# Optimization experiments

Hardware: AMD Instinct MI355X
Metric: run time of the kernel (lower is better)

## Reference

```python
import jax, jax.numpy as jnp
import numpy as np

SEQ, B, IN_DIM = 100, 2048, 64
MID_I, LATENT, V_MID, V_LAT, MID_O, OUT_DIM = 60, 20, 800, 50, 800, 512


def _lstm_cell(x, h, c, wih, whh, bih, bhh):
    # PyTorch gate order: i, f, g, o
    g = x @ wih.T + h @ whh.T + bih + bhh
    i, f, gg, o = jnp.split(g, 4, axis=-1)
    c = jax.nn.sigmoid(f) * c + jax.nn.sigmoid(i) * jnp.tanh(gg)
    h = jax.nn.sigmoid(o) * jnp.tanh(c)
    return h, c


def _lstm_seq(xs, wih, whh, bih, bhh, hid):
    b = xs.shape[1]
    init = (jnp.zeros((b, hid), xs.dtype), jnp.zeros((b, hid), xs.dtype))
    def step(carry, xt):
        h, c = _lstm_cell(xt, carry[0], carry[1], wih, whh, bih, bhh)
        return (h, c), h
    _, outs = jax.lax.scan(step, init, xs)
    return outs  # (seq, B, hid)


def setup_inputs() -> dict:
    key = jax.random.key(0)
    ks = iter(jax.random.split(key, 40))
    w = lambda shape: jax.random.normal(next(ks), shape, jnp.float32) * 0.05
    p = {}
    p['x'] = jax.random.normal(next(ks), (SEQ, B, IN_DIM), jnp.float32)
    p['fc1_wih'] = w((4 * MID_I, IN_DIM)); p['fc1_whh'] = w((4 * MID_I, MID_I))
    p['fc1_bih'] = w((4 * MID_I,)); p['fc1_bhh'] = w((4 * MID_I,))
    p['fc21_wih'] = w((4 * LATENT, MID_I)); p['fc21_whh'] = w((4 * LATENT, LATENT))
    p['fc21_bih'] = w((4 * LATENT,)); p['fc21_bhh'] = w((4 * LATENT,))
    p['lin1_w'] = w((V_MID, LATENT * SEQ)); p['lin1_b'] = w((V_MID,))
    p['lin2_w'] = w((V_LAT, V_MID)); p['lin2_b'] = w((V_LAT,))
    p['idlin_w'] = w((V_LAT, V_LAT)); p['idlin_b'] = w((V_LAT,))
    p['down1_w'] = w((LATENT, V_LAT)); p['down1_b'] = w((LATENT,))
    p['down2_w'] = w((LATENT, OUT_DIM)); p['down2_b'] = w((LATENT,))
    p['l3_wih'] = w((4 * V_LAT, LATENT)); p['l3_whh'] = w((4 * V_LAT, V_LAT))
    p['l3_bih'] = w((4 * V_LAT,)); p['l3_bhh'] = w((4 * V_LAT,))
    p['l4_wih'] = w((4 * MID_O, V_LAT)); p['l4_whh'] = w((4 * MID_O, MID_O))
    p['l4_bih'] = w((4 * MID_O,)); p['l4_bhh'] = w((4 * MID_O,))
    p['l5_wih'] = w((4 * OUT_DIM, MID_O)); p['l5_whh'] = w((4 * OUT_DIM, OUT_DIM))
    p['l5_bih'] = w((4 * OUT_DIM,)); p['l5_bhh'] = w((4 * OUT_DIM,))
    return p


def reference(x, fc1_wih, fc1_whh, fc1_bih, fc1_bhh,
              fc21_wih, fc21_whh, fc21_bih, fc21_bhh,
              lin1_w, lin1_b, lin2_w, lin2_b,
              idlin_w, idlin_b, down1_w, down1_b, down2_w, down2_b,
              l3_wih, l3_whh, l3_bih, l3_bhh,
              l4_wih, l4_whh, l4_bih, l4_bhh,
              l5_wih, l5_whh, l5_bih, l5_bhh):
    seq, b, _ = x.shape
    # encode
    h1 = jax.nn.relu(_lstm_seq(x, fc1_wih, fc1_whh, fc1_bih, fc1_bhh, MID_I))
    out21 = _lstm_seq(h1, fc21_wih, fc21_whh, fc21_bih, fc21_bhh, LATENT)
    flat = jnp.transpose(out21, (1, 2, 0)).reshape(b, -1)  # (B, latent*seq)
    mu = jax.nn.relu(flat @ lin1_w.T + lin1_b)
    mu = jax.nn.relu(mu @ lin2_w.T + lin2_b)  # (B, v_latent)
    # decode
    h_t = mu
    c_t = mu @ idlin_w.T + idlin_b
    out = mu @ down1_w.T + down1_b
    h2 = jnp.zeros((b, MID_O), mu.dtype); c2 = jnp.zeros((b, MID_O), mu.dtype)
    h3 = jnp.zeros((b, OUT_DIM), mu.dtype); c3 = jnp.zeros((b, OUT_DIM), mu.dtype)
    def step(carry, _):
        h_t, c_t, h2, c2, h3, c3, out = carry
        h_t, c_t = _lstm_cell(out, h_t, c_t, l3_wih, l3_whh, l3_bih, l3_bhh)
        h2, c2 = _lstm_cell(h_t, h2, c2, l4_wih, l4_whh, l4_bih, l4_bhh)
        h3, c3 = _lstm_cell(h2, h3, c3, l5_wih, l5_whh, l5_bih, l5_bhh)
        out = h3 @ down2_w.T + down2_b
        return (h_t, c_t, h2, c2, h3, c3, out), h3
    _, muTheta = jax.lax.scan(step, (h_t, c_t, h2, c2, h3, c3, out), None, length=seq)
    return muTheta, mu
```

## Files before the change

kernel.cpp:

```cpp
#include <hip/hip_runtime.h>
#include <cstdint>
#include <cstddef>

#define SEQ     100
#define BATCH   2048
#define IN_DIM  64
#define MID_I   60
#define LATENT  20
#define V_MID   800
#define V_LAT   50
#define MID_O   800
#define OUT_DIM 512

#define KP4  896
#define KP5  1344
#define KPL1 2048

using f32x4  = __attribute__((ext_vector_type(4))) float;
using u16x8  = __attribute__((ext_vector_type(8))) unsigned short;
using bf16x8 = __attribute__((ext_vector_type(8))) __bf16;
typedef _Float16 f16;
typedef _Float16 f16x8 __attribute__((ext_vector_type(8)));

__device__ __forceinline__ unsigned short f2bf(float x){
// ... 41 lines not shown
            for (int i = 0; i < 4; ++i) {
                int idx = threadIdx.x + i * 256;
                int k = idx & 15, m = idx >> 4;
                int gm = m0 + m, gk = k0 + k;
                float v = 0.f;
                if (gm < M && gk < K) v = A[(size_t)gm * K + gk];
                if (RELU_A1 && src == 0) v = fmaxf(v, 0.f);
                As[k][m] = v;
            }
            #pragma unroll
            for (int i = 0; i < 4; ++i) {
                int idx = threadIdx.x + i * 256;
                int k = idx & 15, n = idx >> 4;
                int gn = n0 + n, gk = k0 + k;
                float v = 0.f;
                if (gn < N && gk < K) v = W[(size_t)gn * K + gk];
                Bs[k][n] = v;
            }
            __syncthreads();
            #pragma unroll
            for (int kk = 0; kk < BK; ++kk) {
                float a[4], b[4];
                #pragma unroll
                for (int i = 0; i < 4; ++i) a[i] = As[kk][ty + i * 16];
                #pragma unroll
                for (int j = 0; j < 4; ++j) b[j] = Bs[kk][tx + j * 16];
                #pragma unroll
                for (int i = 0; i < 4; ++i)
                    #pragma unroll
                    for (int j = 0; j < 4; ++j)
                        acc[i][j] += a[i] * b[j];
            }
            __syncthreads();
        }
    }

    #pragma unroll
    for (int i = 0; i < 4; ++i) {
        int gm = m0 + ty + i * 16;
        if (gm >= M) continue;
        #pragma unroll
        for (int j = 0; j < 4; ++j) {
            int gn = n0 + tx + j * 16;
            if (gn >= N) continue;
            float v = acc[i][j];
            if (b1) v += b1[gn];
            if (b2) v += b2[gn];
            if (RELU_OUT) v = fmaxf(v, 0.f);
            C[(size_t)gm * N + gn] = v;
        }
    }
}

__global__ __launch_bounds__(256, 2)
void gemm_lin1(const unsigned short* __restrict__ Ah, const unsigned short* __restrict__ Al,
               const unsigned short* __restrict__ Bh, const unsigned short* __restrict__ Bl,
               int Kp, int Nstore, const float* __restrict__ bi, float* __restrict__ Cout)
{
    __shared__ __align__(16) char smem[32768];
    const int tid  = threadIdx.x;
    const int lane = tid & 63;
    const int wid  = tid >> 6;
    const int m0   = blockIdx.y * 128;
    const int n0   = blockIdx.x * 128;
    const int wr   = (wid >> 1) << 6;
    const int wc   = (wid & 1) << 6;
    const int fr   = lane & 15;
    const int fg   = lane >> 4;
    const int slotR = ((fg ^ (fr & 3)) << 4);

    const int r0 = 32 * wid + (lane >> 2);
    const int sl = (((lane & 3) ^ ((lane >> 2) & 3)) << 3);
    const unsigned short* gA0h = Ah + (size_t)(m0 + r0)      * Kp + sl;
    const unsigned short* gA1h = Ah + (size_t)(m0 + r0 + 16) * Kp + sl;
    const unsigned short* gA0l = Al + (size_t)(m0 + r0)      * Kp + sl;
    const unsigned short* gA1l = Al + (size_t)(m0 + r0 + 16) * Kp + sl;
    const unsigned short* gB0h = Bh + (size_t)(n0 + r0)      * Kp + sl;
    const unsigned short* gB1h = Bh + (size_t)(n0 + r0 + 16) * Kp + sl;
    const unsigned short* gB0l = Bl + (size_t)(n0 + r0)      * Kp + sl;
    const unsigned short* gB1l = Bl + (size_t)(n0 + r0 + 16) * Kp + sl;
    char* lA0h = smem +     0 + (2 * wid    ) * 1024;
    char* lA1h = smem +     0 + (2 * wid + 1) * 1024;
    char* lA0l = smem +  8192 + (2 * wid    ) * 1024;
    char* lA1l = smem +  8192 + (2 * wid + 1) * 1024;
    char* lB0h = smem + 16384 + (2 * wid    ) * 1024;
    char* lB1h = smem + 16384 + (2 * wid + 1) * 1024;
    char* lB0l = smem + 24576 + (2 * wid    ) * 1024;
    char* lB1l = smem + 24576 + (2 * wid + 1) * 1024;

    f32x4 acc[4][4];
    #pragma unroll
    for (int i = 0; i < 4; ++i)
        #pragma unroll
        for (int j = 0; j < 4; ++j) acc[i][j] = (f32x4){0.f, 0.f, 0.f, 0.f};

    for (int k0 = 0; k0 < Kp; k0 += 32) {
        __syncthreads();
        gld16(gA0h + k0, lA0h); gld16(gA1h + k0, lA1h);
        gld16(gA0l + k0, lA0l); gld16(gA1l + k0, lA1l);
        gld16(gB0h + k0, lB0h); gld16(gB1h + k0, lB1h);
        gld16(gB0l + k0, lB0l); gld16(gB1l + k0, lB1l);
        __syncthreads();

        bf16x8 ah[4], al[4];
        #pragma unroll
        for (int i = 0; i < 4; ++i) {
            int ro = (wr + i * 16 + fr) * 64 + slotR;
            ah[i] = *(const bf16x8*)(smem +        ro);
            al[i] = *(const bf16x8*)(smem + 8192 + ro);
        }
        #pragma unroll
        for (int j = 0; j < 4; ++j) {
            int ro = (wc + j * 16 + fr) * 64 + slotR;
            bf16x8 fbh = *(const bf16x8*)(smem + 16384 + ro);
            bf16x8 fbl = *(const bf16x8*)(smem + 24576 + ro);
            #pragma unroll
            for (int i = 0; i < 4; ++i) {
                acc[i][j] = __builtin_amdgcn_mfma_f32_16x16x32_bf16(ah[i], fbh, acc[i][j], 0, 0, 0);
                acc[i][j] = __builtin_amdgcn_mfma_f32_16x16x32_bf16(ah[i], fbl, acc[i][j], 0, 0, 0);
                acc[i][j] = __builtin_amdgcn_mfma_f32_16x16x32_bf16(al[i], fbh, acc[i][j], 0, 0, 0);
            }
        }
    }

    #pragma unroll
    for (int j = 0; j < 4; ++j) {
        int gc = n0 + wc + j * 16 + fr;
        if (gc >= Nstore) continue;
        float badd = bi[gc];
        #pragma unroll
        for (int i = 0; i < 4; ++i)
            #pragma unroll
            for (int r = 0; r < 4; ++r) {
                int gr = m0 + wr + i * 16 + fg * 4 + r;
                float v = fmaxf(acc[i][j][r] + badd, 0.f);
                Cout[(size_t)gr * Nstore + gc] = v;
            }
    }
}

template<int MODE>
__global__ __launch_bounds__(256, 3)
void gemm_dec(const f16* __restrict__ A, const f16* __restrict__ W,
              int Kp, int NK, int H, int NBX,
              const float* __restrict__ bp,
              float* __restrict__ cstate,
              f16* __restrict__ wr1, int st1, int off1,
              f16* __restrict__ wr2, int st2, int off2,
              float* __restrict__ out_t)
{
    __shared__ __align__(16) char smem[49152];
    const int qq      = NBX * 2;
    const int logical = (blockIdx.x & 7) * qq + (blockIdx.x >> 3);
    const int bx = logical >> 4;
    const int by = logical & 15;
    const int m0 = by * 128;
    const int n0 = bx * 128;

    const int tid  = threadIdx.x;
    const int lane = tid & 63;
    const int wid  = tid >> 6;
    const int wm   = wid >> 1;
    const int wn   = wid & 1;
    const int fr   = lane & 15;
    const int fg   = lane >> 4;
    const int swz  = (fg ^ (fr & 3) ^ ((fr >> 2) & 1)) * 16;

    const int rbase = 32 * wid;
    const int lrow  = lane >> 2;
    const int chnk  = (lane & 3) ^ ((lane >> 2) & 3) ^ ((lane >> 4) & 1);
    const f16* sA0 = A + (size_t)(m0 + rbase + lrow)      * Kp + chnk * 8;
    const f16* sA1 = A + (size_t)(m0 + rbase + 16 + lrow) * Kp + chnk * 8;
    const f16* sW0 = W + (size_t)(n0 + rbase + lrow)      * Kp + chnk * 8;
    const f16* sW1 = W + (size_t)(n0 + rbase + 16 + lrow) * Kp + chnk * 8;

    f32x4 acc[4][4];
    #pragma unroll
    for (int i = 0; i < 4; ++i)
        #pragma unroll
        for (int j = 0; j < 4; ++j) acc[i][j] = (f32x4){0.f, 0.f, 0.f, 0.f};

    auto stage = [&](int t, int buf) {
        const int kb = t * 32;
        char* bb = smem + buf * 16384;
        gld16(sA0 + kb, bb + rbase * 64);
        gld16(sA1 + kb, bb + (rbase + 16) * 64);
        gld16(sW0 + kb, bb + 8192 + rbase * 64);
        gld16(sW1 + kb, bb + 8192 + (rbase + 16) * 64);
    };

    stage(0, 0);
    stage(1, 1);

    int buf = 0;
    for (int t = 0; t < NK; ++t) {
        if (t + 1 < NK) asm volatile("s_waitcnt vmcnt(4)" ::: "memory");
        else            asm volatile("s_waitcnt vmcnt(0)" ::: "memory");
        __builtin_amdgcn_s_barrier();
        if (t + 2 < NK) stage(t + 2, (buf + 2) % 3);
        const char* bb = smem + buf * 16384;
        f16x8 af[4];
        #pragma unroll
        for (int i = 0; i < 4; ++i)
            af[i] = *(const f16x8*)(bb + (64 * wm + 16 * i + fr) * 64 + swz);
        #pragma unroll
        for (int j = 0; j < 4; ++j) {
            f16x8 vw = *(const f16x8*)(bb + 8192 + (64 * wn + 16 * j + fr) * 64 + swz);
            #pragma unroll
            for (int i = 0; i < 4; ++i)
                acc[i][j] = __builtin_amdgcn_mfma_f32_16x16x32_f16(af[i], vw, acc[i][j], 0, 0, 0);
        }
        buf = (buf + 1) % 3;
    }

    float* gt = (float*)smem;
    const int u32 = tid & 31;
    const int r8  = tid >> 5;
    const int unit = (n0 >> 2) + u32;
    const f32x4* bp4 = (const f32x4*)bp;
    const f32x4 bv = bp4[unit];

    #pragma unroll
    for (int half = 0; half < 2; ++half) {
        __syncthreads();
        if (wm == half) {
            #pragma unroll
            for (int i = 0; i < 4; ++i)
                #pragma unroll
                for (int j = 0; j < 4; ++j)
                    #pragma unroll
                    for (int r = 0; r < 4; ++r)
                        gt[(16*i + 4*fg + r) * 132 + 64*wn + 16*j + fr] = acc[i][j][r];
        }
        __syncthreads();
        #pragma unroll
        for (int kk = 0; kk < 8; ++kk) {
            const int lr  = 8 * kk + r8;
            const int row = m0 + 64 * half + lr;
            f32x4 g = *(const f32x4*)(gt + lr * 132 + u32 * 4);
            float gi = g[0] + bv[0], gf = g[1] + bv[1];
            float gg = g[2] + bv[2], go = g[3] + bv[3];
            size_t ci = (size_t)row * H + unit;
            float cn = sigm(gf) * cstate[ci] + sigm(gi) * tanh_f(gg);
            float hn = sigm(go) * tanh_f(cn);
            cstate[ci] = cn;
            f16 hh = (f16)hn;
            wr1[(size_t)row * st1 + off1 + unit] = hh;
            if (MODE == 1) wr2[(size_t)row * st2 + off2 + unit] = hh;
            if (MODE == 2) out_t[(size_t)row * H + unit] = hn;
        }
    }
}

__global__ void split_pack_lin1(const float* __restrict__ src,
                                unsigned short* __restrict__ dh, unsigned short* __restrict__ dl)
{
    int idx = blockIdx.x * blockDim.x + threadIdx.x;
    if (idx >= V_MID * LATENT * SEQ) return;
    int n = idx / (LATENT * SEQ), c = idx - n * (LATENT * SEQ);
    int l = c / SEQ, s = c - l * SEQ;
    float x = src[idx];
    unsigned short h = f2bf(x);
    size_t d = (size_t)n * KPL1 + s * LATENT + l;
    dh[d] = h;
    dl[d] = f2bf(x - bf2f(h));
}

__global__ void pack_f16(const float* __restrict__ src, int total, int K, int Kp,
                         int coff, int HU, f16* __restrict__ dh)
{
    int idx = blockIdx.x * blockDim.x + threadIdx.x;
    if (idx >= total) return;
    int n = idx / K, k = idx - n * K;
    int p = (n % HU) * 4 + n / HU;
    dh[(size_t)p * Kp + coff + k] = (f16)src[idx];
}

__global__ void bias_pack(const float* __restrict__ bih, const float* __restrict__ bhh,
                          int H, float* __restrict__ bp)
{
    int idx = blockIdx.x * blockDim.x + threadIdx.x;
    if (idx >= 4 * H) return;
    int g = idx / H, u = idx - g * H;
    bp[u * 4 + g] = bih[idx] + bhh[idx];
}

__global__ __launch_bounds__(256)
void enc_rec1(const float* __restrict__ xp, int T,
              const float* __restrict__ whh,
              float* __restrict__ hbuf, float* __restrict__ cbuf,
              float* __restrict__ h1relu)
{
    __shared__ float Wt[60][240];
    __shared__ float hs[4][60];
    for (int idx = threadIdx.x; idx < 240 * 60; idx += 256) {
        int n = idx / 60, k = idx % 60;
        Wt[k][n] = whh[idx];
    }
    int wid = threadIdx.x >> 6, lane = threadIdx.x & 63;
    int b = blockIdx.x * 4 + wid;
    float h = 0.f, c = 0.f;
    if (lane < 60) {
        h = hbuf[(size_t)b * 60 + lane];
        c = cbuf[(size_t)b * 60 + lane];
        hs[wid][lane] = h;
    }
    __syncthreads();
    for (int t = 0; t < T; ++t) {
        if (lane < 60) {
            const float* xr = xp + ((size_t)t * BATCH + b) * 240;
            float gi = xr[lane], gf = xr[60 + lane], gg = xr[120 + lane], go = xr[180 + lane];
            for (int k = 0; k < 60; ++k) {
                float v = hs[wid][k];
                gi += v * Wt[k][lane];
                gf += v * Wt[k][60 + lane];
                gg += v * Wt[k][120 + lane];
                go += v * Wt[k][180 + lane];
            }
            float cn = sigm(gf) * c + sigm(gi) * tanh_f(gg);
            float hn = sigm(go) * tanh_f(cn);
            c = cn; h = hn;
            h1relu[((size_t)t * BATCH + b) * 60 + lane] = fmaxf(hn, 0.f);
        }
        __syncthreads();
        if (lane < 60) hs[wid][lane] = h;
        __syncthreads();
    }
    if (lane < 60) {
        hbuf[(size_t)b * 60 + lane] = h;
        cbuf[(size_t)b * 60 + lane] = c;
    }
}

__global__ __launch_bounds__(256)
void enc_rec21(const float* __restrict__ xp, int T, int t0,
               const float* __restrict__ whh,
               float* __restrict__ hbuf, float* __restrict__ cbuf,
               unsigned short* __restrict__ fh, unsigned short* __restrict__ fl)
{
    __shared__ float Wt[20][80];
    __shared__ float hs[4][20];
    for (int idx = threadIdx.x; idx < 80 * 20; idx += 256) {
        int n = idx / 20, k = idx % 20;
        Wt[k][n] = whh[idx];
    }
    int wid = threadIdx.x >> 6, lane = threadIdx.x & 63;
    int b = blockIdx.x * 4 + wid;
    float h = 0.f, c = 0.f;
    if (lane < 20) {
        h = hbuf[(size_t)b * 20 + lane];
        c = cbuf[(size_t)b * 20 + lane];
        hs[wid][lane] = h;
    }
    __syncthreads();
    for (int t = 0; t < T; ++t) {
        if (lane < 20) {
            const float* xr = xp + ((size_t)t * BATCH + b) * 80;
            float gi = xr[lane], gf = xr[20 + lane], gg = xr[40 + lane], go = xr[60 + lane];
            for (int k = 0; k < 20; ++k) {
                float v = hs[wid][k];
                gi += v * Wt[k][lane];
                gf += v * Wt[k][20 + lane];
                gg += v * Wt[k][40 + lane];
                go += v * Wt[k][60 + lane];
            }
            float cn = sigm(gf) * c + sigm(gi) * tanh_f(gg);
            float hn = sigm(go) * tanh_f(cn);
            c = cn; h = hn;
            int col = (t0 + t) * 20 + lane;
            unsigned short hh = f2bf(hn);
            fh[(size_t)b * KPL1 + col] = hh;
            fl[(size_t)b * KPL1 + col] = f2bf(hn - bf2f(hh));
        }
        __syncthreads();
        if (lane < 20) hs[wid][lane] = h;
// ... 1 lines not shown
    }
    if (lane < 20) {
        hbuf[(size_t)b * 20 + lane] = h;
        cbuf[(size_t)b * 20 + lane] = c;
    }
}

__global__ __launch_bounds__(256)
void dec_l3(const float* __restrict__ outb,
            const float* __restrict__ wih,
            const float* __restrict__ whh,
            const float* __restrict__ bih, const float* __restrict__ bhh,
            float* __restrict__ h_t, float* __restrict__ c_t,
            f16* __restrict__ a4)
{
    __shared__ float Wt[70][200];
    __shared__ float xin[4][70];
    for (int idx = threadIdx.x; idx < 200 * 20; idx += 256) {
        int n = idx / 20, k = idx % 20;
        Wt[k][n] = wih[idx];
    }
    for (int idx = threadIdx.x; idx < 200 * 50; idx += 256) {
        int n = idx / 50, k = idx % 50;
        Wt[20 + k][n] = whh[idx];
    }
    int wid = threadIdx.x >> 6, lane = threadIdx.x & 63;
    int b = blockIdx.x * 4 + wid;
    if (lane < 20) xin[wid][lane]      = outb[(size_t)b * 20 + lane];
    if (lane < 50) xin[wid][20 + lane] = h_t[(size_t)b * 50 + lane];
    __syncthreads();
    if (lane < 50) {
        float gi = bih[lane] + bhh[lane];
        float gf = bih[50 + lane] + bhh[50 + lane];
        float gg = bih[100 + lane] + bhh[100 + lane];
        float go = bih[150 + lane] + bhh[150 + lane];
        for (int k = 0; k < 70; ++k) {
            float v = xin[wid][k];
            gi += v * Wt[k][lane];
            gf += v * Wt[k][50 + lane];
            gg += v * Wt[k][100 + lane];
            go += v * Wt[k][150 + lane];
        }
        float cold = c_t[(size_t)b * 50 + lane];
        float cn = sigm(gf) * cold + sigm(gi) * tanh_f(gg);
        float hn = sigm(go) * tanh_f(cn);
        c_t[(size_t)b * 50 + lane] = cn;
        h_t[(size_t)b * 50 + lane] = hn;
        a4[(size_t)b * KP4 + lane] = (f16)hn;
    }
}

__global__ __launch_bounds__(512)
void dec_step3(const float* __restrict__ h3prev,
               const float* __restrict__ w2, const float* __restrict__ b2,
               const float* __restrict__ wih, const float* __restrict__ whh,
               const float* __restrict__ bih, const float* __restrict__ bhh,
               float* __restrict__ h_t, float* __restrict__ c_t,
               f16* __restrict__ a4)
{
    __shared__ float w2s[20][512];
    __shared__ float W3[70][200];
    __shared__ float xb[8][80];
    const int tid  = threadIdx.x;
    const int lane = tid & 63;
    const int w    = tid >> 6;
    const int row  = blockIdx.x * 8 + w;

    for (int idx = tid; idx < 20 * 512; idx += 512)
        w2s[idx >> 9][idx & 511] = w2[idx];
    for (int idx = tid; idx < 200 * 20; idx += 512) {
        int n = idx / 20, k = idx - n * 20;
        W3[k][n] = wih[idx];
    }
    for (int idx = tid; idx < 200 * 50; idx += 512) {
        int n = idx / 50, k = idx - n * 50;
        W3[20 + k][n] = whh[idx];
    }
    if (lane < 50) xb[w][20 + lane] = h_t[(size_t)row * 50 + lane];

    float hreg[8];
    const float* hrow = h3prev + (size_t)row * 512;
    #pragma unroll
    for (int c = 0; c < 8; ++c) hreg[c] = hrow[lane + 64 * c];
    __syncthreads();

    #pragma unroll 4
    for (int n = 0; n < 20; ++n) {
        float s = 0.f;
        #pragma unroll
        for (int c = 0; c < 8; ++c) s += hreg[c] * w2s[n][lane + 64 * c];
        #pragma unroll
        for (int o = 32; o; o >>= 1) s += __shfl_xor(s, o);
        if (lane == 0) xb[w][n] = s + b2[n];
    }
    __syncthreads();

    if (lane < 50) {
        const int u = lane;
        float gi = bih[u] + bhh[u];
        float gf = bih[50 + u] + bhh[50 + u];
        float gg = bih[100 + u] + bhh[100 + u];
        float go = bih[150 + u] + bhh[150 + u];
        for (int k = 0; k < 70; ++k) {
            float v = xb[w][k];
            gi += v * W3[k][u];
            gf += v * W3[k][50 + u];
            gg += v * W3[k][100 + u];
            go += v * W3[k][150 + u];
        }
        size_t ci = (size_t)row * 50 + u;
        float cn = sigm(gf) * c_t[ci] + sigm(gi) * tanh_f(gg);
        float hn = sigm(go) * tanh_f(cn);
        c_t[ci] = cn;
        h_t[ci] = hn;
        a4[(size_t)row * KP4 + u] = (f16)hn;
    }
}

extern "C" void kernel_launch(void* const* d_in, const int* in_sizes, int n_in,
                              void* d_out_v, int out_size, void* d_ws, size_t ws_size,
                              hipStream_t stream)
{
    const float* x        = (const float*)d_in[0];
    const float* fc1_wih  = (const float*)d_in[1];
    const float* fc1_whh  = (const float*)d_in[2];
    const float* fc1_bih  = (const float*)d_in[3];
    const float* fc1_bhh  = (const float*)d_in[4];
    const float* fc21_wih = (const float*)d_in[5];
    const float* fc21_whh = (const float*)d_in[6];
    const float* fc21_bih = (const float*)d_in[7];
    const float* fc21_bhh = (const float*)d_in[8];
    const float* lin1_w   = (const float*)d_in[9];
    const float* lin1_b   = (const float*)d_in[10];
    const float* lin2_w   = (const float*)d_in[11];
    const float* lin2_b   = (const float*)d_in[12];
    const float* idlin_w  = (const float*)d_in[13];
    const float* idlin_b  = (const float*)d_in[14];
    const float* down1_w  = (const float*)d_in[15];
    const float* down1_b  = (const float*)d_in[16];
    const float* down2_w  = (const float*)d_in[17];
    const float* down2_b  = (const float*)d_in[18];
    const float* l3_wih   = (const float*)d_in[19];
    const float* l3_whh   = (const float*)d_in[20];
    const float* l3_bih   = (const float*)d_in[21];
    const float* l3_bhh   = (const float*)d_in[22];
    const float* l4_wih   = (const float*)d_in[23];
    const float* l4_whh   = (const float*)d_in[24];
    const float* l4_bih   = (const float*)d_in[25];
    const float* l4_bhh   = (const float*)d_in[26];
    const float* l5_wih   = (const float*)d_in[27];
    const float* l5_whh   = (const float*)d_in[28];
    const float* l5_bih   = (const float*)d_in[29];
    const float* l5_bhh   = (const float*)d_in[30];
    float* out = (float*)d_out_v;

    char* base = (char*)d_ws;
    size_t off = 0;
    auto alloc = [&](size_t bytes) -> void* {
        off = (off + 255) & ~(size_t)255;
        void* p = base + off;
        off += bytes;
        return p;
    };

    size_t us_begin = (off + 255) & ~(size_t)255;
    f16* W4h = (f16*)alloc((size_t)3200 * KP4 * 2);
    f16* W5h = (f16*)alloc((size_t)2048 * KP5 * 2);
    unsigned short* L1h = (unsigned short*)alloc((size_t)896 * KPL1 * 2);
    unsigned short* L1l = (unsigned short*)alloc((size_t)896 * KPL1 * 2);
    unsigned short* Fh  = (unsigned short*)alloc((size_t)BATCH * KPL1 * 2);
    unsigned short* Fl  = (unsigned short*)alloc((size_t)BATCH * KPL1 * 2);
    f16* A4[2]; f16* A5[2];
    for (int p = 0; p < 2; ++p) {
        A4[p] = (f16*)alloc((size_t)BATCH * KP4 * 2);
        A5[p] = (f16*)alloc((size_t)BATCH * KP5 * 2);
    }
    size_t us_end = off;

    size_t fz_begin = (off + 255) & ~(size_t)255;
    float* c2   = (float*)alloc((size_t)BATCH * MID_O * 4);
    float* c3   = (float*)alloc((size_t)BATCH * OUT_DIM * 4);
    float* hb1  = (float*)alloc((size_t)BATCH * MID_I * 4);
    float* cb1  = (float*)alloc((size_t)BATCH * MID_I * 4);
    float* hb21 = (float*)alloc((size_t)BATCH * LATENT * 4);
    float* cb21 = (float*)alloc((size_t)BATCH * LATENT * 4);
    size_t fz_end = off;

    float* bp4   = (float*)alloc((size_t)4 * MID_O * 4);
    float* bp5   = (float*)alloc((size_t)4 * OUT_DIM * 4);
    float* mu1   = (float*)alloc((size_t)BATCH * V_MID * 4);
    float* mu    = (float*)alloc((size_t)BATCH * V_LAT * 4);
    float* h_t   = (float*)alloc((size_t)BATCH * V_LAT * 4);
    float* c_t   = (float*)alloc((size_t)BATCH * V_LAT * 4);
    float* outb  = (float*)alloc((size_t)BATCH * LATENT * 4);
    const int CH = 20;
    float* xp1c  = (float*)alloc((size_t)CH * BATCH * 4 * MID_I * 4);
    float* h1rc  = (float*)alloc((size_t)CH * BATCH * MID_I * 4);
    float* xp21c = (float*)alloc((size_t)CH * BATCH * 4 * LATENT * 4);

    hipMemsetAsync(base + us_begin, 0, us_end - us_begin, stream);
    hipMemsetAsync(base + fz_begin, 0, fz_end - fz_begin, stream);

    pack_f16<<<(3200 * 50  + 255) / 256, 256, 0, stream>>>(l4_wih, 3200 * 50,  50,  KP4, 0,   800, W4h);
    pack_f16<<<(3200 * 800 + 255) / 256, 256, 0, stream>>>(l4_whh, 3200 * 800, 800, KP4, 64,  800, W4h);
    pack_f16<<<(2048 * 800 + 255) / 256, 256, 0, stream>>>(l5_wih, 2048 * 800, 800, KP5, 0,   512, W5h);
    pack_f16<<<(2048 * 512 + 255) / 256, 256, 0, stream>>>(l5_whh, 2048 * 512, 512, KP5, 832, 512, W5h);
    split_pack_lin1<<<(V_MID * LATENT * SEQ + 255) / 256, 256, 0, stream>>>(lin1_w, L1h, L1l);
    bias_pack<<<(4 * MID_O   + 255) / 256, 256, 0, stream>>>(l4_bih, l4_bhh, MID_O,   bp4);
    bias_pack<<<(4 * OUT_DIM + 255) / 256, 256, 0, stream>>>(l5_bih, l5_bhh, OUT_DIM, bp5);

    for (int c0 = 0; c0 < SEQ; c0 += CH) {
        {
            dim3 g((4 * MID_I + BN - 1) / BN, CH * BATCH / BM);
            gemm2k<false, false><<<g, 256, 0, stream>>>(
                x + (size_t)c0 * BATCH * IN_DIM, IN_DIM, nullptr, 0,
                fc1_wih, nullptr, fc1_bih, fc1_bhh, xp1c, CH * BATCH, 4 * MID_I);
        }
        enc_rec1<<<BATCH / 4, 256, 0, stream>>>(xp1c, CH, fc1_whh, hb1, cb1, h1rc);
        {
            dim3 g((4 * LATENT + BN - 1) / BN, CH * BATCH / BM);
            gemm2k<false, false><<<g, 256, 0, stream>>>(
                h1rc, MID_I, nullptr, 0,
                fc21_wih, nullptr, fc21_bih, fc21_bhh, xp21c, CH * BATCH, 4 * LATENT);
        }
        enc_rec21<<<BATCH / 4, 256, 0, stream>>>(xp21c, CH, c0, fc21_whh, hb21, cb21, Fh, Fl);
    }

    {
        dim3 g(7, 16);
        gemm_lin1<<<g, 256, 0, stream>>>(Fh, Fl, L1h, L1l, KPL1, V_MID, lin1_b, mu1);
    }
    {
        dim3 g((V_LAT + BN - 1) / BN, BATCH / BM);
        gemm2k<false, true><<<g, 256, 0, stream>>>(mu1, V_MID, nullptr, 0,
            lin2_w, nullptr, lin2_b, nullptr, mu, BATCH, V_LAT);
    }

    hipMemcpyAsync(h_t, mu, (size_t)BATCH * V_LAT * 4, hipMemcpyDeviceToDevice, stream);
    {
        dim3 g(1, BATCH / BM);
        gemm2k<false, false><<<g, 256, 0, stream>>>(mu, V_LAT, nullptr, 0,
            idlin_w, nullptr, idlin_b, nullptr, c_t, BATCH, V_LAT);
        gemm2k<false, false><<<g, 256, 0, stream>>>(mu, V_LAT, nullptr, 0,
            down1_w, nullptr, down1_b, nullptr, outb, BATCH, LATENT);
    }

    for (int t = 0; t < SEQ; ++t) {
        const int p = t & 1;
        if (t == 0) {
            dec_l3<<<BATCH / 4, 256, 0, stream>>>(outb, l3_wih, l3_whh, l3_bih, l3_bhh,
                                                  h_t, c_t, A4[0]);
        } else {
            dec_step3<<<BATCH / 8, 512, 0, stream>>>(
                out + (size_t)(t - 1) * BATCH * OUT_DIM,
                down2_w, down2_b, l3_wih, l3_whh, l3_bih, l3_bhh,
                h_t, c_t, A4[p]);
        }
        {
            gemm_dec<1><<<dim3(400), 256, 0, stream>>>(
                A4[p], W4h, KP4, KP4 / 32, MID_O, 25, bp4, c2,
                A4[p ^ 1], KP4, 64,
                A5[p], KP5, 0,
                nullptr);
        }
        {
            gemm_dec<2><<<dim3(256), 256, 0, stream>>>(
                A5[p], W5h, KP5, KP5 / 32, OUT_DIM, 16, bp5, c3,
                A5[p ^ 1], KP5, 832,
                nullptr, 0, 0,
                out + (size_t)t * BATCH * OUT_DIM);
        }
    }

    hipMemcpyAsync(out + (size_t)SEQ * BATCH * OUT_DIM, mu,
                   (size_t)BATCH * V_LAT * 4, hipMemcpyDeviceToDevice, stream);
}
```

Measured before the change: 7.671 ms.

## Use split-bf16 MFMA for encoder input GEMMs and retile layer-4 decoder GEMM

The encoder input projections for fc1 and fc21 now run on a generalized split-bf16 (hi/lo) MFMA GEMM instead of the scalar gemm2k. Inputs, weights and the relu'd h1 are pre-split into bf16 pairs, and the two biases are pre-summed. The decoder layer-4 GEMM is retiled to 256x128 blocks with 512 threads and 200 blocks, which halves redundant weight loads per block but uses more LDS and gives fewer blocks. The down2 weight is also stored as f16 in LDS inside dec_step3, which adds small precision loss in the output feedback.

```diff
diff --git a/kernel.cpp b/kernel.cpp
--- a/kernel.cpp
+++ b/kernel.cpp
@@ -117,10 +117,11 @@
     }
 }
 
+template<bool RELU>
 __global__ __launch_bounds__(256, 2)
-void gemm_lin1(const unsigned short* __restrict__ Ah, const unsigned short* __restrict__ Al,
-               const unsigned short* __restrict__ Bh, const unsigned short* __restrict__ Bl,
-               int Kp, int Nstore, const float* __restrict__ bi, float* __restrict__ Cout)
+void gemm_mfma0(const unsigned short* __restrict__ Ah, const unsigned short* __restrict__ Al,
+                const unsigned short* __restrict__ Bh, const unsigned short* __restrict__ Bl,
+                int Kp, int Nstore, const float* __restrict__ bi, float* __restrict__ Cout)
 {
     __shared__ __align__(16) char smem[32768];
     const int tid  = threadIdx.x;
@@ -198,28 +199,26 @@
             #pragma unroll
             for (int r = 0; r < 4; ++r) {
                 int gr = m0 + wr + i * 16 + fg * 4 + r;
-                float v = fmaxf(acc[i][j][r] + badd, 0.f);
+                float v = acc[i][j][r] + badd;
+                if (RELU) v = fmaxf(v, 0.f);
                 Cout[(size_t)gr * Nstore + gc] = v;
             }
     }
 }
 
-template<int MODE>
-__global__ __launch_bounds__(256, 3)
-void gemm_dec(const f16* __restrict__ A, const f16* __restrict__ W,
-              int Kp, int NK, int H, int NBX,
-              const float* __restrict__ bp,
-              float* __restrict__ cstate,
-              f16* __restrict__ wr1, int st1, int off1,
-              f16* __restrict__ wr2, int st2, int off2,
-              float* __restrict__ out_t)
-{
-    __shared__ __align__(16) char smem[49152];
-    const int qq      = NBX * 2;
+__global__ __launch_bounds__(512, 2)
+void gemm_dec4(const f16* __restrict__ A, const f16* __restrict__ W,
+               int Kp, int NK, int H, int NBX,
+               const float* __restrict__ bp, float* __restrict__ cstate,
+               f16* __restrict__ wr1, int st1, int off1,
+               f16* __restrict__ wr2, int st2, int off2)
+{
+    __shared__ __align__(16) char smem[73728];
+    const int qq      = NBX;
     const int logical = (blockIdx.x & 7) * qq + (blockIdx.x >> 3);
-    const int bx = logical >> 4;
-    const int by = logical & 15;
-    const int m0 = by * 128;
+    const int bx = logical >> 3;
+    const int by = logical & 7;
+    const int m0 = by * 256;
     const int n0 = bx * 128;
 
     const int tid  = threadIdx.x;
@@ -232,6 +231,113 @@
     const int swz  = (fg ^ (fr & 3) ^ ((fr >> 2) & 1)) * 16;
 
     const int rbase = 32 * wid;
+    const int rbW   = 16 * wid;
+    const int lrow  = lane >> 2;
+    const int chnk  = (lane & 3) ^ ((lane >> 2) & 3) ^ ((lane >> 4) & 1);
+    const f16* sA0 = A + (size_t)(m0 + rbase + lrow)      * Kp + chnk * 8;
+    const f16* sA1 = A + (size_t)(m0 + rbase + 16 + lrow) * Kp + chnk * 8;
+    const f16* sW  = W + (size_t)(n0 + rbW + lrow)        * Kp + chnk * 8;
+
+    f32x4 acc[4][4];
+    #pragma unroll
+    for (int i = 0; i < 4; ++i)
+        #pragma unroll
+        for (int j = 0; j < 4; ++j) acc[i][j] = (f32x4){0.f, 0.f, 0.f, 0.f};
+
+    auto stage = [&](int t, int buf) {
+        const int kb = t * 32;
+        char* bb = smem + buf * 24576;
+        gld16(sA0 + kb, bb + rbase * 64);
+        gld16(sA1 + kb, bb + (rbase + 16) * 64);
+        gld16(sW  + kb, bb + 16384 + rbW * 64);
+    };
+
+    stage(0, 0);
+    stage(1, 1);
+
+    int buf = 0;
+    for (int t = 0; t < NK; ++t) {
+        if (t + 1 < NK) asm volatile("s_waitcnt vmcnt(3)" ::: "memory");
+        else            asm volatile("s_waitcnt vmcnt(0)" ::: "memory");
+        __builtin_amdgcn_s_barrier();
+        if (t + 2 < NK) stage(t + 2, (buf + 2) % 3);
+        const char* bb = smem + buf * 24576;
+        f16x8 af[4];
+        #pragma unroll
+        for (int i = 0; i < 4; ++i)
+            af[i] = *(const f16x8*)(bb + (64 * wm + 16 * i + fr) * 64 + swz);
+        #pragma unroll
+        for (int j = 0; j < 4; ++j) {
+            f16x8 vw = *(const f16x8*)(bb + 16384 + (64 * wn + 16 * j + fr) * 64 + swz);
+            #pragma unroll
+            for (int i = 0; i < 4; ++i)
+                acc[i][j] = __builtin_amdgcn_mfma_f32_16x16x32_f16(af[i], vw, acc[i][j], 0, 0, 0);
+        }
+        buf = (buf + 1) % 3;
+    }
+
+    float* gt = (float*)smem;
+    const int u32 = tid & 31;
+    const int rr  = tid >> 5;
+    const int unit = (n0 >> 2) + u32;
+    const f32x4 bv = ((const f32x4*)bp)[unit];
+
+    #pragma unroll
+    for (int qp = 0; qp < 4; ++qp) {
+        __syncthreads();
+        if (wm == qp) {
+            #pragma unroll
+            for (int i = 0; i < 4; ++i)
+                #pragma unroll
+                for (int j = 0; j < 4; ++j)
+                    #pragma unroll
+                    for (int r = 0; r < 4; ++r)
+                        gt[(16*i + 4*fg + r) * 132 + 64*wn + 16*j + fr] = acc[i][j][r];
+        }
+        __syncthreads();
+        #pragma unroll
+        for (int kk = 0; kk < 4; ++kk) {
+            const int lr  = 16 * kk + rr;
+            const int row = m0 + 64 * qp + lr;
+            f32x4 g = *(const f32x4*)(gt + lr * 132 + u32 * 4);
+            float gi = g[0] + bv[0], gf = g[1] + bv[1];
+            float gg = g[2] + bv[2], go = g[3] + bv[3];
+            size_t ci = (size_t)row * H + unit;
+            float cn = sigm(gf) * cstate[ci] + sigm(gi) * tanh_f(gg);
+            float hn = sigm(go) * tanh_f(cn);
+            cstate[ci] = cn;
+            f16 hh = (f16)hn;
+            wr1[(size_t)row * st1 + off1 + unit] = hh;
+            wr2[(size_t)row * st2 + off2 + unit] = hh;
+        }
+    }
+}
+
+__global__ __launch_bounds__(256, 3)
+void gemm_dec5(const f16* __restrict__ A, const f16* __restrict__ W,
+               int Kp, int NK, int H, int NBX,
+               const float* __restrict__ bp, float* __restrict__ cstate,
+               f16* __restrict__ wr1, int st1, int off1,
+               float* __restrict__ out_t)
+{
+    __shared__ __align__(16) char smem[49152];
+    const int qq      = NBX * 2;
+    const int logical = (blockIdx.x & 7) * qq + (blockIdx.x >> 3);
+    const int bx = logical >> 4;
+    const int by = logical & 15;
+    const int m0 = by * 128;
+    const int n0 = bx * 128;
+
+    const int tid  = threadIdx.x;
+    const int lane = tid & 63;
+    const int wid  = tid >> 6;
+    const int wm   = wid >> 1;
+    const int wn   = wid & 1;
+    const int fr   = lane & 15;
+    const int fg   = lane >> 4;
+    const int swz  = (fg ^ (fr & 3) ^ ((fr >> 2) & 1)) * 16;
+
+    const int rbase = 32 * wid;
     const int lrow  = lane >> 2;
     const int chnk  = (lane & 3) ^ ((lane >> 2) & 3) ^ ((lane >> 4) & 1);
     const f16* sA0 = A + (size_t)(m0 + rbase + lrow)      * Kp + chnk * 8;
@@ -282,8 +388,7 @@
     const int u32 = tid & 31;
     const int r8  = tid >> 5;
     const int unit = (n0 >> 2) + u32;
-    const f32x4* bp4 = (const f32x4*)bp;
-    const f32x4 bv = bp4[unit];
+    const f32x4 bv = ((const f32x4*)bp)[unit];
 
     #pragma unroll
     for (int half = 0; half < 2; ++half) {
@@ -309,10 +414,8 @@
             float cn = sigm(gf) * cstate[ci] + sigm(gi) * tanh_f(gg);
             float hn = sigm(go) * tanh_f(cn);
             cstate[ci] = cn;
-            f16 hh = (f16)hn;
-            wr1[(size_t)row * st1 + off1 + unit] = hh;
-            if (MODE == 1) wr2[(size_t)row * st2 + off2 + unit] = hh;
-            if (MODE == 2) out_t[(size_t)row * H + unit] = hn;
+            wr1[(size_t)row * st1 + off1 + unit] = (f16)hn;
+            out_t[(size_t)row * H + unit] = hn;
         }
     }
 }
@@ -331,6 +434,19 @@
     dl[d] = f2bf(x - bf2f(h));
 }
 
+__global__ void split_pack_rows(const float* __restrict__ src, int total, int K, int Kp,
+                                unsigned short* __restrict__ dh, unsigned short* __restrict__ dl)
+{
+    int idx = blockIdx.x * blockDim.x + threadIdx.x;
+    if (idx >= total) return;
+    int n = idx / K, k = idx - n * K;
+    float x = src[idx];
+    unsigned short h = f2bf(x);
+    size_t d = (size_t)n * Kp + k;
+    dh[d] = h;
+    dl[d] = f2bf(x - bf2f(h));
+}
+
 __global__ void pack_f16(const float* __restrict__ src, int total, int K, int Kp,
                          int coff, int HU, f16* __restrict__ dh)
 {
@@ -341,6 +457,12 @@
     dh[(size_t)p * Kp + coff + k] = (f16)src[idx];
 }
 
+__global__ void pack_flat_f16(const float* __restrict__ src, int total, f16* __restrict__ d)
+{
+    int idx = blockIdx.x * blockDim.x + threadIdx.x;
+    if (idx < total) d[idx] = (f16)src[idx];
+}
+
 __global__ void bias_pack(const float* __restrict__ bih, const float* __restrict__ bhh,
                           int H, float* __restrict__ bp)
 {
@@ -350,11 +472,18 @@
     bp[u * 4 + g] = bih[idx] + bhh[idx];
 }
 
+__global__ void bias_sum(const float* __restrict__ a, const float* __restrict__ b,
+                         int n, float* __restrict__ d)
+{
+    int idx = blockIdx.x * blockDim.x + threadIdx.x;
+    if (idx < n) d[idx] = a[idx] + b[idx];
+}
+
 __global__ __launch_bounds__(256)
 void enc_rec1(const float* __restrict__ xp, int T,
               const float* __restrict__ whh,
               float* __restrict__ hbuf, float* __restrict__ cbuf,
-              float* __restrict__ h1relu)
+              unsigned short* __restrict__ h1h, unsigned short* __restrict__ h1l)
 {
     __shared__ float Wt[60][240];
     __shared__ float hs[4][60];
@@ -385,7 +514,11 @@
             float cn = sigm(gf) * c + sigm(gi) * tanh_f(gg);
             float hn = sigm(go) * tanh_f(cn);
             c = cn; h = hn;
-            h1relu[((size_t)t * BATCH + b) * 60 + lane] = fmaxf(hn, 0.f);
+            float rh = fmaxf(hn, 0.f);
+            unsigned short hh = f2bf(rh);
+            size_t d = ((size_t)t * BATCH + b) * 64 + lane;
+            h1h[d] = hh;
+            h1l[d] = f2bf(rh - bf2f(hh));
         }
         __syncthreads();
         if (lane < 60) hs[wid][lane] = h;
@@ -493,13 +626,13 @@
 
 __global__ __launch_bounds__(512)
 void dec_step3(const float* __restrict__ h3prev,
-               const float* __restrict__ w2, const float* __restrict__ b2,
+               const f16* __restrict__ w2p, const float* __restrict__ b2,
                const float* __restrict__ wih, const float* __restrict__ whh,
                const float* __restrict__ bih, const float* __restrict__ bhh,
                float* __restrict__ h_t, float* __restrict__ c_t,
                f16* __restrict__ a4)
 {
-    __shared__ float w2s[20][512];
+    __shared__ f16   w2s[20][512];
     __shared__ float W3[70][200];
     __shared__ float xb[8][80];
     const int tid  = threadIdx.x;
@@ -508,7 +641,7 @@
     const int row  = blockIdx.x * 8 + w;
 
     for (int idx = tid; idx < 20 * 512; idx += 512)
-        w2s[idx >> 9][idx & 511] = w2[idx];
+        w2s[idx >> 9][idx & 511] = w2p[idx];
     for (int idx = tid; idx < 200 * 20; idx += 512) {
         int n = idx / 20, k = idx - n * 20;
         W3[k][n] = wih[idx];
@@ -529,7 +662,7 @@
     for (int n = 0; n < 20; ++n) {
         float s = 0.f;
         #pragma unroll
-        for (int c = 0; c < 8; ++c) s += hreg[c] * w2s[n][lane + 64 * c];
+        for (int c = 0; c < 8; ++c) s += hreg[c] * (float)w2s[n][lane + 64 * c];
         #pragma unroll
         for (int o = 32; o; o >>= 1) s += __shfl_xor(s, o);
         if (lane == 0) xb[w][n] = s + b2[n];
@@ -611,6 +744,13 @@
     unsigned short* L1l = (unsigned short*)alloc((size_t)896 * KPL1 * 2);
     unsigned short* Fh  = (unsigned short*)alloc((size_t)BATCH * KPL1 * 2);
     unsigned short* Fl  = (unsigned short*)alloc((size_t)BATCH * KPL1 * 2);
+    unsigned short* Fc1h  = (unsigned short*)alloc((size_t)256 * 64 * 2);
+    unsigned short* Fc1l  = (unsigned short*)alloc((size_t)256 * 64 * 2);
+    unsigned short* Fc21h = (unsigned short*)alloc((size_t)128 * 64 * 2);
+    unsigned short* Fc21l = (unsigned short*)alloc((size_t)128 * 64 * 2);
+    const int CH = 20;
+    unsigned short* H1h = (unsigned short*)alloc((size_t)CH * BATCH * 64 * 2);
+    unsigned short* H1l = (unsigned short*)alloc((size_t)CH * BATCH * 64 * 2);
     f16* A4[2]; f16* A5[2];
     for (int p = 0; p < 2; ++p) {
         A4[p] = (f16*)alloc((size_t)BATCH * KP4 * 2);
@@ -629,14 +769,17 @@
 
     float* bp4   = (float*)alloc((size_t)4 * MID_O * 4);
     float* bp5   = (float*)alloc((size_t)4 * OUT_DIM * 4);
+    float* bs1   = (float*)alloc((size_t)4 * MID_I * 4);
+    float* bs21  = (float*)alloc((size_t)4 * LATENT * 4);
+    f16*   w2p   = (f16*)alloc((size_t)LATENT * OUT_DIM * 2);
     float* mu1   = (float*)alloc((size_t)BATCH * V_MID * 4);
     float* mu    = (float*)alloc((size_t)BATCH * V_LAT * 4);
     float* h_t   = (float*)alloc((size_t)BATCH * V_LAT * 4);
     float* c_t   = (float*)alloc((size_t)BATCH * V_LAT * 4);
     float* outb  = (float*)alloc((size_t)BATCH * LATENT * 4);
-    const int CH = 20;
+    unsigned short* Xh = (unsigned short*)alloc((size_t)SEQ * BATCH * 64 * 2);
+    unsigned short* Xl = (unsigned short*)alloc((size_t)SEQ * BATCH * 64 * 2);
     float* xp1c  = (float*)alloc((size_t)CH * BATCH * 4 * MID_I * 4);
-    float* h1rc  = (float*)alloc((size_t)CH * BATCH * MID_I * 4);
     float* xp21c = (float*)alloc((size_t)CH * BATCH * 4 * LATENT * 4);
 
     hipMemsetAsync(base + us_begin, 0, us_end - us_begin, stream);
@@ -647,29 +790,34 @@
     pack_f16<<<(2048 * 800 + 255) / 256, 256, 0, stream>>>(l5_wih, 2048 * 800, 800, KP5, 0,   512, W5h);
     pack_f16<<<(2048 * 512 + 255) / 256, 256, 0, stream>>>(l5_whh, 2048 * 512, 512, KP5, 832, 512, W5h);
     split_pack_lin1<<<(V_MID * LATENT * SEQ + 255) / 256, 256, 0, stream>>>(lin1_w, L1h, L1l);
+    split_pack_rows<<<(240 * 64 + 255) / 256, 256, 0, stream>>>(fc1_wih, 240 * 64, 64, 64, Fc1h, Fc1l);
+    split_pack_rows<<<(80 * 60 + 255) / 256, 256, 0, stream>>>(fc21_wih, 80 * 60, 60, 64, Fc21h, Fc21l);
+    split_pack_rows<<<(SEQ * BATCH * 64 + 255) / 256, 256, 0, stream>>>(x, SEQ * BATCH * 64, 64, 64, Xh, Xl);
+    pack_flat_f16<<<(LATENT * OUT_DIM + 255) / 256, 256, 0, stream>>>(down2_w, LATENT * OUT_DIM, w2p);
     bias_pack<<<(4 * MID_O   + 255) / 256, 256, 0, stream>>>(l4_bih, l4_bhh, MID_O,   bp4);
     bias_pack<<<(4 * OUT_DIM + 255) / 256, 256, 0, stream>>>(l5_bih, l5_bhh, OUT_DIM, bp5);
+    bias_sum<<<1, 256, 0, stream>>>(fc1_bih, fc1_bhh, 4 * MID_I, bs1);
+    bias_sum<<<1, 256, 0, stream>>>(fc21_bih, fc21_bhh, 4 * LATENT, bs21);
 
     for (int c0 = 0; c0 < SEQ; c0 += CH) {
         {
-            dim3 g((4 * MID_I + BN - 1) / BN, CH * BATCH / BM);
-            gemm2k<false, false><<<g, 256, 0, stream>>>(
-                x + (size_t)c0 * BATCH * IN_DIM, IN_DIM, nullptr, 0,
-                fc1_wih, nullptr, fc1_bih, fc1_bhh, xp1c, CH * BATCH, 4 * MID_I);
-        }
-        enc_rec1<<<BATCH / 4, 256, 0, stream>>>(xp1c, CH, fc1_whh, hb1, cb1, h1rc);
+            dim3 g(2, CH * BATCH / 128);
+            gemm_mfma0<false><<<g, 256, 0, stream>>>(
+                Xh + (size_t)c0 * BATCH * 64, Xl + (size_t)c0 * BATCH * 64,
+                Fc1h, Fc1l, 64, 4 * MID_I, bs1, xp1c);
+        }
+        enc_rec1<<<BATCH / 4, 256, 0, stream>>>(xp1c, CH, fc1_whh, hb1, cb1, H1h, H1l);
         {
-            dim3 g((4 * LATENT + BN - 1) / BN, CH * BATCH / BM);
-            gemm2k<false, false><<<g, 256, 0, stream>>>(
-                h1rc, MID_I, nullptr, 0,
-                fc21_wih, nullptr, fc21_bih, fc21_bhh, xp21c, CH * BATCH, 4 * LATENT);
+            dim3 g(1, CH * BATCH / 128);
+            gemm_mfma0<false><<<g, 256, 0, stream>>>(
+                H1h, H1l, Fc21h, Fc21l, 64, 4 * LATENT, bs21, xp21c);
         }
         enc_rec21<<<BATCH / 4, 256, 0, stream>>>(xp21c, CH, c0, fc21_whh, hb21, cb21, Fh, Fl);
     }
 
     {
         dim3 g(7, 16);
-        gemm_lin1<<<g, 256, 0, stream>>>(Fh, Fl, L1h, L1l, KPL1, V_MID, lin1_b, mu1);
+        gemm_mfma0<true><<<g, 256, 0, stream>>>(Fh, Fl, L1h, L1l, KPL1, V_MID, lin1_b, mu1);
     }
     {
         dim3 g((V_LAT + BN - 1) / BN, BATCH / BM);
@@ -694,21 +842,19 @@
         } else {
             dec_step3<<<BATCH / 8, 512, 0, stream>>>(
                 out + (size_t)(t - 1) * BATCH * OUT_DIM,
-                down2_w, down2_b, l3_wih, l3_whh, l3_bih, l3_bhh,
+                w2p, down2_b, l3_wih, l3_whh, l3_bih, l3_bhh,
                 h_t, c_t, A4[p]);
         }
         {
-            gemm_dec<1><<<dim3(400), 256, 0, stream>>>(
+            gemm_dec4<<<dim3(200), 512, 0, stream>>>(
                 A4[p], W4h, KP4, KP4 / 32, MID_O, 25, bp4, c2,
                 A4[p ^ 1], KP4, 64,
-                A5[p], KP5, 0,
-                nullptr);
+                A5[p], KP5, 0);
         }
         {
-            gemm_dec<2><<<dim3(256), 256, 0, stream>>>(
+            gemm_dec5<<<dim3(256), 256, 0, stream>>>(
                 A5[p], W5h, KP5, KP5 / 32, OUT_DIM, 16, bp5, c3,
                 A5[p ^ 1], KP5, 832,
-                nullptr, 0, 0,
                 out + (size_t)t * BATCH * OUT_DIM);
         }
     }
```

After: 7.555 ms. Within noise of the previous version (-1.5%).

## Use split-bf16 MFMA GEMM for encoder input projections and remap decoder XCD tiling

Applied to the files above, without the earlier changes.

Replaces the scalar gemm2k input projections of both encoder LSTMs with the split-bf16 MFMA kernel (generalized from gemm_lin1). The inputs, weights and the relu'd h1 output are pre-split into hi/lo bf16 pairs padded to K=64, and the biases are pre-summed. The decoder GEMM block-to-XCD mapping now gives each XCD a contiguous band of row tiles for better L2 reuse of the A operand. down2_w is stored as f16 in shared memory in dec_step3, which halves its LDS footprint but loses precision. The change adds preprocessing passes over x and extra buffers.

```diff
diff --git a/kernel.cpp b/kernel.cpp
--- a/kernel.cpp
+++ b/kernel.cpp
@@ -117,10 +117,11 @@
     }
 }
 
+template<bool RELU>
 __global__ __launch_bounds__(256, 2)
-void gemm_lin1(const unsigned short* __restrict__ Ah, const unsigned short* __restrict__ Al,
-               const unsigned short* __restrict__ Bh, const unsigned short* __restrict__ Bl,
-               int Kp, int Nstore, const float* __restrict__ bi, float* __restrict__ Cout)
+void gemm_mfma0(const unsigned short* __restrict__ Ah, const unsigned short* __restrict__ Al,
+                const unsigned short* __restrict__ Bh, const unsigned short* __restrict__ Bl,
+                int Kp, int Nstore, const float* __restrict__ bi, float* __restrict__ Cout)
 {
     __shared__ __align__(16) char smem[32768];
     const int tid  = threadIdx.x;
@@ -198,7 +199,8 @@
             #pragma unroll
             for (int r = 0; r < 4; ++r) {
                 int gr = m0 + wr + i * 16 + fg * 4 + r;
-                float v = fmaxf(acc[i][j][r] + badd, 0.f);
+                float v = acc[i][j][r] + badd;
+                if (RELU) v = fmaxf(v, 0.f);
                 Cout[(size_t)gr * Nstore + gc] = v;
             }
     }
@@ -207,7 +209,7 @@
 template<int MODE>
 __global__ __launch_bounds__(256, 3)
 void gemm_dec(const f16* __restrict__ A, const f16* __restrict__ W,
-              int Kp, int NK, int H, int NBX,
+              int Kp, int NK, int H, int NBYX,
               const float* __restrict__ bp,
               float* __restrict__ cstate,
               f16* __restrict__ wr1, int st1, int off1,
@@ -215,10 +217,10 @@
               float* __restrict__ out_t)
 {
     __shared__ __align__(16) char smem[49152];
-    const int qq      = NBX * 2;
-    const int logical = (blockIdx.x & 7) * qq + (blockIdx.x >> 3);
-    const int bx = logical >> 4;
-    const int by = logical & 15;
+    const int xcd = blockIdx.x & 7;
+    const int ii  = blockIdx.x >> 3;
+    const int by  = xcd * NBYX + (ii % NBYX);
+    const int bx  = ii / NBYX;
     const int m0 = by * 128;
     const int n0 = bx * 128;
 
@@ -282,8 +284,7 @@
     const int u32 = tid & 31;
     const int r8  = tid >> 5;
     const int unit = (n0 >> 2) + u32;
-    const f32x4* bp4 = (const f32x4*)bp;
-    const f32x4 bv = bp4[unit];
+    const f32x4 bv = ((const f32x4*)bp)[unit];
 
     #pragma unroll
     for (int half = 0; half < 2; ++half) {
@@ -331,6 +332,19 @@
     dl[d] = f2bf(x - bf2f(h));
 }
 
+__global__ void split_pack_rows(const float* __restrict__ src, int total, int K, int Kp,
+                                unsigned short* __restrict__ dh, unsigned short* __restrict__ dl)
+{
+    int idx = blockIdx.x * blockDim.x + threadIdx.x;
+    if (idx >= total) return;
+    int n = idx / K, k = idx - n * K;
+    float x = src[idx];
+    unsigned short h = f2bf(x);
+    size_t d = (size_t)n * Kp + k;
+    dh[d] = h;
+    dl[d] = f2bf(x - bf2f(h));
+}
+
 __global__ void pack_f16(const float* __restrict__ src, int total, int K, int Kp,
                          int coff, int HU, f16* __restrict__ dh)
 {
@@ -341,6 +355,12 @@
     dh[(size_t)p * Kp + coff + k] = (f16)src[idx];
 }
 
+__global__ void pack_flat_f16(const float* __restrict__ src, int total, f16* __restrict__ d)
+{
+    int idx = blockIdx.x * blockDim.x + threadIdx.x;
+    if (idx < total) d[idx] = (f16)src[idx];
+}
+
 __global__ void bias_pack(const float* __restrict__ bih, const float* __restrict__ bhh,
                           int H, float* __restrict__ bp)
 {
@@ -350,11 +370,18 @@
     bp[u * 4 + g] = bih[idx] + bhh[idx];
 }
 
+__global__ void bias_sum(const float* __restrict__ a, const float* __restrict__ b,
+                         int n, float* __restrict__ d)
+{
+    int idx = blockIdx.x * blockDim.x + threadIdx.x;
+    if (idx < n) d[idx] = a[idx] + b[idx];
+}
+
 __global__ __launch_bounds__(256)
 void enc_rec1(const float* __restrict__ xp, int T,
               const float* __restrict__ whh,
               float* __restrict__ hbuf, float* __restrict__ cbuf,
-              float* __restrict__ h1relu)
+              unsigned short* __restrict__ h1h, unsigned short* __restrict__ h1l)
 {
     __shared__ float Wt[60][240];
     __shared__ float hs[4][60];
@@ -385,7 +412,11 @@
             float cn = sigm(gf) * c + sigm(gi) * tanh_f(gg);
             float hn = sigm(go) * tanh_f(cn);
             c = cn; h = hn;
-            h1relu[((size_t)t * BATCH + b) * 60 + lane] = fmaxf(hn, 0.f);
+            float rh = fmaxf(hn, 0.f);
+            unsigned short hh = f2bf(rh);
+            size_t d = ((size_t)t * BATCH + b) * 64 + lane;
+            h1h[d] = hh;
+            h1l[d] = f2bf(rh - bf2f(hh));
         }
         __syncthreads();
         if (lane < 60) hs[wid][lane] = h;
@@ -493,13 +524,13 @@
 
 __global__ __launch_bounds__(512)
 void dec_step3(const float* __restrict__ h3prev,
-               const float* __restrict__ w2, const float* __restrict__ b2,
+               const f16* __restrict__ w2p, const float* __restrict__ b2,
                const float* __restrict__ wih, const float* __restrict__ whh,
                const float* __restrict__ bih, const float* __restrict__ bhh,
                float* __restrict__ h_t, float* __restrict__ c_t,
                f16* __restrict__ a4)
 {
-    __shared__ float w2s[20][512];
+    __shared__ f16   w2s[20][512];
     __shared__ float W3[70][200];
     __shared__ float xb[8][80];
     const int tid  = threadIdx.x;
@@ -508,7 +539,7 @@
     const int row  = blockIdx.x * 8 + w;
 
     for (int idx = tid; idx < 20 * 512; idx += 512)
-        w2s[idx >> 9][idx & 511] = w2[idx];
+        w2s[idx >> 9][idx & 511] = w2p[idx];
     for (int idx = tid; idx < 200 * 20; idx += 512) {
         int n = idx / 20, k = idx - n * 20;
         W3[k][n] = wih[idx];
@@ -529,7 +560,7 @@
     for (int n = 0; n < 20; ++n) {
         float s = 0.f;
         #pragma unroll
-        for (int c = 0; c < 8; ++c) s += hreg[c] * w2s[n][lane + 64 * c];
+        for (int c = 0; c < 8; ++c) s += hreg[c] * (float)w2s[n][lane + 64 * c];
         #pragma unroll
         for (int o = 32; o; o >>= 1) s += __shfl_xor(s, o);
         if (lane == 0) xb[w][n] = s + b2[n];
@@ -611,6 +642,13 @@
     unsigned short* L1l = (unsigned short*)alloc((size_t)896 * KPL1 * 2);
     unsigned short* Fh  = (unsigned short*)alloc((size_t)BATCH * KPL1 * 2);
     unsigned short* Fl  = (unsigned short*)alloc((size_t)BATCH * KPL1 * 2);
+    unsigned short* Fc1h  = (unsigned short*)alloc((size_t)256 * 64 * 2);
+    unsigned short* Fc1l  = (unsigned short*)alloc((size_t)256 * 64 * 2);
+    unsigned short* Fc21h = (unsigned short*)alloc((size_t)128 * 64 * 2);
+    unsigned short* Fc21l = (unsigned short*)alloc((size_t)128 * 64 * 2);
+    const int CH = 20;
+    unsigned short* H1h = (unsigned short*)alloc((size_t)CH * BATCH * 64 * 2);
+    unsigned short* H1l = (unsigned short*)alloc((size_t)CH * BATCH * 64 * 2);
     f16* A4[2]; f16* A5[2];
     for (int p = 0; p < 2; ++p) {
         A4[p] = (f16*)alloc((size_t)BATCH * KP4 * 2);
@@ -629,14 +667,17 @@
 
     float* bp4   = (float*)alloc((size_t)4 * MID_O * 4);
     float* bp5   = (float*)alloc((size_t)4 * OUT_DIM * 4);
+    float* bs1   = (float*)alloc((size_t)4 * MID_I * 4);
+    float* bs21  = (float*)alloc((size_t)4 * LATENT * 4);
+    f16*   w2p   = (f16*)alloc((size_t)LATENT * OUT_DIM * 2);
     float* mu1   = (float*)alloc((size_t)BATCH * V_MID * 4);
     float* mu    = (float*)alloc((size_t)BATCH * V_LAT * 4);
     float* h_t   = (float*)alloc((size_t)BATCH * V_LAT * 4);
     float* c_t   = (float*)alloc((size_t)BATCH * V_LAT * 4);
     float* outb  = (float*)alloc((size_t)BATCH * LATENT * 4);
-    const int CH = 20;
+    unsigned short* Xh = (unsigned short*)alloc((size_t)SEQ * BATCH * 64 * 2);
+    unsigned short* Xl = (unsigned short*)alloc((size_t)SEQ * BATCH * 64 * 2);
     float* xp1c  = (float*)alloc((size_t)CH * BATCH * 4 * MID_I * 4);
-    float* h1rc  = (float*)alloc((size_t)CH * BATCH * MID_I * 4);
     float* xp21c = (float*)alloc((size_t)CH * BATCH * 4 * LATENT * 4);
 
     hipMemsetAsync(base + us_begin, 0, us_end - us_begin, stream);
@@ -647,29 +688,34 @@
     pack_f16<<<(2048 * 800 + 255) / 256, 256, 0, stream>>>(l5_wih, 2048 * 800, 800, KP5, 0,   512, W5h);
     pack_f16<<<(2048 * 512 + 255) / 256, 256, 0, stream>>>(l5_whh, 2048 * 512, 512, KP5, 832, 512, W5h);
     split_pack_lin1<<<(V_MID * LATENT * SEQ + 255) / 256, 256, 0, stream>>>(lin1_w, L1h, L1l);
+    split_pack_rows<<<(240 * 64 + 255) / 256, 256, 0, stream>>>(fc1_wih, 240 * 64, 64, 64, Fc1h, Fc1l);
+    split_pack_rows<<<(80 * 60 + 255) / 256, 256, 0, stream>>>(fc21_wih, 80 * 60, 60, 64, Fc21h, Fc21l);
+    split_pack_rows<<<(SEQ * BATCH * 64 + 255) / 256, 256, 0, stream>>>(x, SEQ * BATCH * 64, 64, 64, Xh, Xl);
+    pack_flat_f16<<<(LATENT * OUT_DIM + 255) / 256, 256, 0, stream>>>(down2_w, LATENT * OUT_DIM, w2p);
     bias_pack<<<(4 * MID_O   + 255) / 256, 256, 0, stream>>>(l4_bih, l4_bhh, MID_O,   bp4);
     bias_pack<<<(4 * OUT_DIM + 255) / 256, 256, 0, stream>>>(l5_bih, l5_bhh, OUT_DIM, bp5);
+    bias_sum<<<1, 256, 0, stream>>>(fc1_bih, fc1_bhh, 4 * MID_I, bs1);
+    bias_sum<<<1, 256, 0, stream>>>(fc21_bih, fc21_bhh, 4 * LATENT, bs21);
 
     for (int c0 = 0; c0 < SEQ; c0 += CH) {
         {
-            dim3 g((4 * MID_I + BN - 1) / BN, CH * BATCH / BM);
-            gemm2k<false, false><<<g, 256, 0, stream>>>(
-                x + (size_t)c0 * BATCH * IN_DIM, IN_DIM, nullptr, 0,
-                fc1_wih, nullptr, fc1_bih, fc1_bhh, xp1c, CH * BATCH, 4 * MID_I);
-        }
-        enc_rec1<<<BATCH / 4, 256, 0, stream>>>(xp1c, CH, fc1_whh, hb1, cb1, h1rc);
+            dim3 g(2, CH * BATCH / 128);
+            gemm_mfma0<false><<<g, 256, 0, stream>>>(
+                Xh + (size_t)c0 * BATCH * 64, Xl + (size_t)c0 * BATCH * 64,
+                Fc1h, Fc1l, 64, 4 * MID_I, bs1, xp1c);
+        }
+        enc_rec1<<<BATCH / 4, 256, 0, stream>>>(xp1c, CH, fc1_whh, hb1, cb1, H1h, H1l);
         {
-            dim3 g((4 * LATENT + BN - 1) / BN, CH * BATCH / BM);
-            gemm2k<false, false><<<g, 256, 0, stream>>>(
-                h1rc, MID_I, nullptr, 0,
-                fc21_wih, nullptr, fc21_bih, fc21_bhh, xp21c, CH * BATCH, 4 * LATENT);
+            dim3 g(1, CH * BATCH / 128);
+            gemm_mfma0<false><<<g, 256, 0, stream>>>(
+                H1h, H1l, Fc21h, Fc21l, 64, 4 * LATENT, bs21, xp21c);
         }
         enc_rec21<<<BATCH / 4, 256, 0, stream>>>(xp21c, CH, c0, fc21_whh, hb21, cb21, Fh, Fl);
     }
 
     {
         dim3 g(7, 16);
-        gemm_lin1<<<g, 256, 0, stream>>>(Fh, Fl, L1h, L1l, KPL1, V_MID, lin1_b, mu1);
+        gemm_mfma0<true><<<g, 256, 0, stream>>>(Fh, Fl, L1h, L1l, KPL1, V_MID, lin1_b, mu1);
     }
     {
         dim3 g((V_LAT + BN - 1) / BN, BATCH / BM);
@@ -694,19 +740,19 @@
         } else {
             dec_step3<<<BATCH / 8, 512, 0, stream>>>(
                 out + (size_t)(t - 1) * BATCH * OUT_DIM,
-                down2_w, down2_b, l3_wih, l3_whh, l3_bih, l3_bhh,
+                w2p, down2_b, l3_wih, l3_whh, l3_bih, l3_bhh,
                 h_t, c_t, A4[p]);
         }
         {
             gemm_dec<1><<<dim3(400), 256, 0, stream>>>(
-                A4[p], W4h, KP4, KP4 / 32, MID_O, 25, bp4, c2,
+                A4[p], W4h, KP4, KP4 / 32, MID_O, 2, bp4, c2,
                 A4[p ^ 1], KP4, 64,
                 A5[p], KP5, 0,
                 nullptr);
         }
         {
             gemm_dec<2><<<dim3(256), 256, 0, stream>>>(
-                A5[p], W5h, KP5, KP5 / 32, OUT_DIM, 16, bp5, c3,
+                A5[p], W5h, KP5, KP5 / 32, OUT_DIM, 2, bp5, c3,
                 A5[p ^ 1], KP5, 832,
                 nullptr, 0, 0,
                 out + (size_t)t * BATCH * OUT_DIM);
```

Result: faster. 7.518 ms (-2.0%).
